# Kernel tuning notes

Measured on AMD Instinct MI355X. Metric: run time of the kernel, lower is better.

The kernel has to match this reference:

```python
import jax, jax.numpy as jnp
import numpy as np

WS = 8            # window size
OWIN = 12         # overlapping window: int(8*0.5)+8
HEADS = 4
DHEAD = 16
INNER = 64        # HEADS*DHEAD
DIM = 48
B, H, W = 4, 192, 192
HN, WN = H // WS, W // WS
NW = HN * WN
NK = NW // 2      # deterministic hard-token keep count (ratio=0.5, E[gumbel rate]=0.5)
SCALE = DHEAD ** -0.5


def conv1x1(x, w, b=None):
    y = jnp.einsum('bchw,oc->bohw', x, w)
    return y if b is None else y + b[:, None, None]


def win_part(x):
    # 'b c (h dh) (w dw) -> b (h w) (dh dw) c'
    b, c, h, w = x.shape
    x = x.reshape(b, c, h // WS, WS, w // WS, WS).transpose(0, 2, 4, 3, 5, 1)
    return x.reshape(b, (h // WS) * (w // WS), WS * WS, c)


def win_unpart(x, h, w):
    b, n, l, c = x.shape
    x = x.reshape(b, h // WS, w // WS, WS, WS, c).transpose(0, 5, 1, 3, 2, 4)
    return x.reshape(b, c, h, w)


def unfold_overlap(x):
    # nn.Unfold(kernel=OWIN, stride=WS, pad=(OWIN-WS)//2) -> (b, NW, OWIN^2, c)
    pad = (OWIN - WS) // 2
    xp = jnp.pad(x, ((0, 0), (0, 0), (pad, pad), (pad, pad)))
    hi = (jnp.arange(HN) * WS)[:, None] + jnp.arange(OWIN)[None]
    wi = (jnp.arange(WN) * WS)[:, None] + jnp.arange(OWIN)[None]
    p = xp[:, :, hi[:, None, :, None], wi[None, :, None, :]]  # (b,c,HN,WN,OWIN,OWIN)
    b, c = x.shape[:2]
    return p.reshape(b, c, NW, OWIN * OWIN).transpose(0, 2, 3, 1)


def rel_to_abs(x):
    b, l, m = x.shape
    r = (m + 1) // 2
    x = jnp.pad(x, ((0, 0), (0, 0), (0, 1)))
    flat = jnp.pad(x.reshape(b, l * (m + 1)), ((0, 0), (0, m - l)))
    return flat.reshape(b, l + 1, m)[:, :l, m - r:]


def relative_logits_1d(q, rel_k):
    b, h, w, d = q.shape
    r = (rel_k.shape[0] + 1) // 2
    logits = jnp.einsum('bxyd,rd->bxyr', q, rel_k)
    logits = rel_to_abs(logits.reshape(b * h, w, -1)).reshape(b, h, w, r)
    return jnp.broadcast_to(logits[:, :, None, :, :], (b, h, r, w, r))


def rel_pos_emb(q, rel_h, rel_w):
    # q: (B_, WS*WS, d) -> (B_, WS*WS, OWIN*OWIN)
    B_, L, d = q.shape
    q4 = q.reshape(B_, WS, WS, d)
    lw = relative_logits_1d(q4, rel_w).transpose(0, 1, 3, 2, 4).reshape(B_, L, -1)
    lh = relative_logits_1d(q4.transpose(0, 2, 1, 3), rel_h).transpose(0, 3, 1, 4, 2).reshape(B_, L, -1)
    return lw + lh


def reference(x, condition_global, wq, bq, wk, bk, wv, bv, w_in, b_in, ln_w, ln_b,
              w_sa, b_sa, w_m1, b_m1, w_m2, b_m2, rel_h, rel_w, w_out, b_out):
    b = x.shape[0]
    qs = conv1x1(x, wq, bq)
    ks = conv1x1(x, wk, bk)
    vs = conv1x1(x, wv, bv)

    # deformable condition: per-window normalized coordinate grid
    lin = jnp.linspace(-1.0, 1.0, WS, dtype=x.dtype)
    gy, gx = jnp.meshgrid(lin, lin, indexing='ij')
    wind = jnp.tile(jnp.stack([gy, gx]), (1, HN, WN))
    cond = jnp.concatenate([vs, condition_global, jnp.broadcast_to(wind, (b, 2, H, W))], axis=1)

    # PredictorLG (inference routing)
    t = conv1x1(cond, w_in, b_in)
    mu = t.mean(1, keepdims=True)
    var = ((t - mu) ** 2).mean(1, keepdims=True)
    t = (t - mu) / jnp.sqrt(var + 1e-6)
    t = t * ln_w[:, None, None] + ln_b[:, None, None]
    t = jax.nn.leaky_relu(t, 0.1)
    sa = jax.nn.sigmoid(jax.lax.conv_general_dilated(
        t, w_sa, (1, 1), ((1, 1), (1, 1)),
        dimension_numbers=('NCHW', 'OIHW', 'NCHW')) + b_sa[:, None, None])
    m = win_part(t.mean(1, keepdims=True)).reshape(b, NW, WS * WS)
    h1 = jax.nn.leaky_relu(m @ w_m1.T + b_m1, 0.1)
    pred = jax.nn.softmax(h1 @ w_m2.T + b_m2, axis=-1)
    score = pred[:, :, 0]
    order = jnp.argsort(-score, axis=1)
    idx1, idx2 = order[:, :NK], order[:, NK:]

    # hard branch: gather -> overlapping window attention with rel-pos bias
    qw = jnp.take_along_axis(win_part(qs), idx1[:, :, None, None], axis=1)       # (b,NK,WS^2,INNER)
    kw = jnp.take_along_axis(unfold_overlap(ks), idx1[:, :, None, None], axis=1)  # (b,NK,OWIN^2,INNER)
    vw = jnp.take_along_axis(unfold_overlap(vs), idx1[:, :, None, None], axis=1)
    qh = qw.reshape(b, NK, WS * WS, HEADS, DHEAD)
    kh = kw.reshape(b, NK, OWIN * OWIN, HEADS, DHEAD)
    vh = vw.reshape(b, NK, OWIN * OWIN, HEADS, DHEAD)
    sim = SCALE * jnp.einsum('bnqhd,bnkhd->bnhqk', qh, kh)
    rp = rel_pos_emb(qh.transpose(0, 1, 3, 2, 4).reshape(b * NK * HEADS, WS * WS, DHEAD), rel_h, rel_w)
    sim = sim + rp.reshape(b, NK, HEADS, WS * WS, OWIN * OWIN)
    attn = jax.nn.softmax(sim, axis=-1)
    hard = jnp.einsum('bnhqk,bnkhd->bnqhd', attn, vh).reshape(b, NK, WS * WS, INNER)

    # easy branch: spatial-attention-gated values
    easy = jnp.take_along_axis(win_part(vs * sa), idx2[:, :, None, None], axis=1)

    # scatter-merge (batch_index_fill)
    bar = jnp.arange(b)[:, None]
    merged = jnp.zeros((b, NW, WS * WS, INNER), x.dtype)
    merged = merged.at[bar, idx1].set(hard).at[bar, idx2].set(easy)
    out = win_unpart(merged, H, W)
    return conv1x1(out, w_out, b_out)


def setup_inputs() -> dict:
    key = jax.random.key(0)
    k = jax.random.split(key, 16)
    rn = lambda kk, s, sc=0.05: jax.random.normal(kk, s, jnp.float32) * sc
    return {
        'x': jax.random.normal(k[0], (B, DIM, H, W), jnp.float32),
        'condition_global': jax.random.normal(k[1], (B, 2, H, W), jnp.float32),
        'wq': rn(k[2], (INNER, DIM)), 'bq': jnp.zeros((INNER,), jnp.float32),
        'wk': rn(k[3], (INNER, DIM)), 'bk': jnp.zeros((INNER,), jnp.float32),
        'wv': rn(k[4], (INNER, DIM)), 'bv': jnp.zeros((INNER,), jnp.float32),
        'w_in': rn(k[5], (17, 68)), 'b_in': jnp.zeros((17,), jnp.float32),
        'ln_w': jnp.ones((17,), jnp.float32), 'ln_b': jnp.zeros((17,), jnp.float32),
        'w_sa': rn(k[6], (1, 17, 3, 3)), 'b_sa': jnp.zeros((1,), jnp.float32),
        'w_m1': rn(k[7], (WS, WS * WS)), 'b_m1': jnp.zeros((WS,), jnp.float32),
        'w_m2': rn(k[8], (2, WS)), 'b_m2': jnp.zeros((2,), jnp.float32),
        'rel_h': rn(k[9], (2 * OWIN - 1, DHEAD), DHEAD ** -0.5),
        'rel_w': rn(k[10], (2 * OWIN - 1, DHEAD), DHEAD ** -0.5),
        'w_out': rn(k[11], (DIM, INNER)), 'b_out': jnp.zeros((DIM,), jnp.float32),
    }
```

## Files before the change

### kernel.cpp

```cpp
#include <hip/hip_runtime.h>
#include <math.h>

#define Hh 192
#define Ww 192
#define HWc 36864
#define Bc 4
#define NWc 576
#define NKc 288
#define WNc 24

typedef _Float16 h2_t __attribute__((ext_vector_type(2)));
typedef _Float16 f16x4 __attribute__((ext_vector_type(4)));
typedef float f32x4 __attribute__((ext_vector_type(4)));
typedef unsigned u32x2 __attribute__((ext_vector_type(2)));
__device__ __forceinline__ h2_t u2h(unsigned u) { return __builtin_bit_cast(h2_t, u); }
__device__ __forceinline__ unsigned h2u(h2_t h) { return __builtin_bit_cast(unsigned, h); }
__device__ __forceinline__ h2_t pkrtz(float a, float b) {
    return __builtin_bit_cast(h2_t, __builtin_amdgcn_cvt_pkrtz(a, b));
}
__device__ __forceinline__ f16x4 pk4(float4 v) {
    u32x2 p = { h2u(pkrtz(v.x, v.y)), h2u(pkrtz(v.z, v.w)) };
    return __builtin_bit_cast(f16x4, p);
}
#define L2E 1.44269504f

__global__ __launch_bounds__(256, 1) void k_qkv(const float* __restrict__ x,
    const float* __restrict__ wq, const float* __restrict__ bq,
    const float* __restrict__ wk, const float* __restrict__ bk,
    const float* __restrict__ wvw, const float* __restrict__ bv,
    _Float16* __restrict__ q, _Float16* __restrict__ k, float* __restrict__ v)
{
    __shared__ float xs[132][52];

    int tid = threadIdx.x;
    int blk = blockIdx.x;
    int b = blk / 288;
    int g0 = (blk % 288) * 128;
    const float* xb = x + (size_t)b * 48 * HWc + g0;

    #pragma unroll
    for (int it = 0; it < 24; ++it) {
        int i = it * 256 + tid;
        int c = i >> 7, px = i & 127;
        xs[px][c] = xb[(size_t)c * HWc + px];
    }

    int ln = tid & 63, wave = tid >> 6;
    int dgrp = ln >> 4;
    __syncthreads();

    size_t pbase = (size_t)b * HWc + g0;

    {
        f16x4 Aq[4][3], Ak[4][3];
        #pragma unroll
        for (int ot = 0; ot < 4; ++ot)
            #pragma unroll
            for (int ks = 0; ks < 3; ++ks) {
                int oc = ot * 16 + (ln & 15);
                Aq[ot][ks] = pk4(*(const float4*)(wq + oc * 48 + ks * 16 + dgrp * 4));
                Ak[ot][ks] = pk4(*(const float4*)(wk + oc * 48 + ks * 16 + dgrp * 4));
            }
        float4 bqf[4], bkf[4];
        #pragma unroll
        for (int ot = 0; ot < 4; ++ot) {
            bqf[ot] = *(const float4*)(bq + ot * 16 + dgrp * 4);
            bkf[ot] = *(const float4*)(bk + ot * 16 + dgrp * 4);
        }

        #pragma unroll
        for (int t2 = 0; t2 < 2; ++t2) {
            int tn = wave * 2 + t2;
            int px = tn * 16 + (ln & 15);
            f16x4 Bf[3];
            #pragma unroll
            for (int ks = 0; ks < 3; ++ks)
                Bf[ks] = pk4(*(const float4*)&xs[px][ks * 16 + dgrp * 4]);

            #pragma unroll
            for (int ot = 0; ot < 4; ++ot) {
                f32x4 Dq = { bqf[ot].x, bqf[ot].y, bqf[ot].z, bqf[ot].w };
                f32x4 Dk = { bkf[ot].x, bkf[ot].y, bkf[ot].z, bkf[ot].w };
                #pragma unroll
                for (int ks = 0; ks < 3; ++ks) {
                    Dq = __builtin_amdgcn_mfma_f32_16x16x16f16(Aq[ot][ks], Bf[ks], Dq, 0, 0, 0);
                    Dk = __builtin_amdgcn_mfma_f32_16x16x16f16(Ak[ot][ks], Bf[ks], Dk, 0, 0, 0);
                }
                u32x2 q2 = { h2u(pkrtz(Dq[0], Dq[1])), h2u(pkrtz(Dq[2], Dq[3])) };
                u32x2 k2 = { h2u(pkrtz(Dk[0], Dk[1])), h2u(pkrtz(Dk[2], Dk[3])) };
                size_t off = (pbase + (size_t)px) * 64 + ot * 16 + dgrp * 4;
                *(u32x2*)(q + off) = q2;
                *(u32x2*)(k + off) = k2;
            }
        }
    }

    {
        float4 Wv[12];
        #pragma unroll
        for (int j = 0; j < 12; ++j) Wv[j] = *(const float4*)(wvw + ln * 48 + j * 4);
        float bvv = bv[ln];

        int p0 = wave * 32;
        #pragma unroll 1
        for (int g4 = 0; g4 < 8; ++g4) {
            int px = p0 + g4 * 4;
            float a0 = bvv, a1 = bvv, a2 = bvv, a3 = bvv;
            #pragma unroll
            for (int j = 0; j < 12; ++j) {
                float4 x0 = *(const float4*)&xs[px + 0][j * 4];
                float4 x1 = *(const float4*)&xs[px + 1][j * 4];
                float4 x2 = *(const float4*)&xs[px + 2][j * 4];
                float4 x3 = *(const float4*)&xs[px + 3][j * 4];
                a0 = fmaf(x0.x, Wv[j].x, a0); a0 = fmaf(x0.y, Wv[j].y, a0);
                a0 = fmaf(x0.z, Wv[j].z, a0); a0 = fmaf(x0.w, Wv[j].w, a0);
                a1 = fmaf(x1.x, Wv[j].x, a1); a1 = fmaf(x1.y, Wv[j].y, a1);
                a1 = fmaf(x1.z, Wv[j].z, a1); a1 = fmaf(x1.w, Wv[j].w, a1);
                a2 = fmaf(x2.x, Wv[j].x, a2); a2 = fmaf(x2.y, Wv[j].y, a2);
                a2 = fmaf(x2.z, Wv[j].z, a2); a2 = fmaf(x2.w, Wv[j].w, a2);
                a3 = fmaf(x3.x, Wv[j].x, a3); a3 = fmaf(x3.y, Wv[j].y, a3);
                a3 = fmaf(x3.z, Wv[j].z, a3); a3 = fmaf(x3.w, Wv[j].w, a3);
            }
            v[(pbase + (size_t)(px + 0)) * 64 + ln] = a0;
            v[(pbase + (size_t)(px + 1)) * 64 + ln] = a1;
            v[(pbase + (size_t)(px + 2)) * 64 + ln] = a2;
            v[(pbase + (size_t)(px + 3)) * 64 + ln] = a3;
        }
    }
}

__global__ __launch_bounds__(256) void k_cond(const float* __restrict__ vs,
    const float* __restrict__ cg,
    const float* __restrict__ w_in, const float* __restrict__ b_in,
    const float* __restrict__ ln_w, const float* __restrict__ ln_b,
    float* __restrict__ t, float* __restrict__ mpix)
{
    int g = blockIdx.x * 256 + threadIdx.x;
    int b = g / HWc, rem = g % HWc;
    int y = rem / Ww, xx = rem % Ww;

    float in[68];
    const float* vp = vs + (size_t)g * 64;
    #pragma unroll
    for (int c = 0; c < 64; c += 4) {
        float4 t4 = *(const float4*)(vp + c);
        in[c] = t4.x; in[c+1] = t4.y; in[c+2] = t4.z; in[c+3] = t4.w;
    }
    in[64] = cg[((size_t)b * 2 + 0) * HWc + rem];
    in[65] = cg[((size_t)b * 2 + 1) * HWc + rem];
    const float step = 2.0f / 7.0f;
    in[66] = -1.0f + step * (float)(y & 7);
    in[67] = -1.0f + step * (float)(xx & 7);

    float tv[17];
    float mu = 0.f;
    #pragma unroll
    for (int o = 0; o < 17; ++o) {
        float a = b_in[o];
        const float* wr = w_in + o * 68;
        #pragma unroll
        for (int c = 0; c < 68; ++c) a = fmaf(in[c], wr[c], a);
        tv[o] = a;
        mu += a;
    }
    mu *= (1.f / 17.f);
    float var = 0.f;
    #pragma unroll
    for (int o = 0; o < 17; ++o) { float d = tv[o] - mu; var = fmaf(d, d, var); }
    var *= (1.f / 17.f);
    float rstd = 1.f / sqrtf(var + 1e-6f);

    float msum = 0.f;
    #pragma unroll
    for (int o = 0; o < 17; ++o) {
        float z = (tv[o] - mu) * rstd * ln_w[o] + ln_b[o];
        z = (z >= 0.f) ? z : 0.1f * z;
        t[((size_t)b * 17 + o) * HWc + rem] = z;
        msum += z;
    }
    mpix[(size_t)b * HWc + rem] = msum * (1.f / 17.f);
}

__global__ __launch_bounds__(256) void k_sa(const float* __restrict__ t,
    const float* __restrict__ w_sa, const float* __restrict__ b_sa,
    float* __restrict__ sa)
{
    int g = blockIdx.x * 256 + threadIdx.x;
    int b = g / HWc, rem = g % HWc;
    int y = rem / Ww, xx = rem % Ww;

    float a = b_sa[0];
    for (int c = 0; c < 17; ++c) {
        const float* tp = t + ((size_t)b * 17 + c) * HWc;
        const float* wr = w_sa + c * 9;
        #pragma unroll
        for (int ki = 0; ki < 3; ++ki) {
            int yy = y + ki - 1;
            if ((unsigned)yy >= 192u) continue;
            #pragma unroll
            for (int kj = 0; kj < 3; ++kj) {
                int xc = xx + kj - 1;
                if ((unsigned)xc >= 192u) continue;
                a = fmaf(tp[yy * Ww + xc], wr[ki * 3 + kj], a);
            }
        }
    }
    sa[g] = 1.f / (1.f + expf(-a));
}

__global__ __launch_bounds__(576) void k_score(const float* __restrict__ mpix,
    const float* __restrict__ w_m1, const float* __restrict__ b_m1,
    const float* __restrict__ w_m2, const float* __restrict__ b_m2,
    int* __restrict__ hardl, int* __restrict__ easyl)
{
    __shared__ float sc[NWc];
    int b = blockIdx.x;
    int w = threadIdx.x;
    {
        int hy = w / WNc, wx = w % WNc;
        const float* mp = mpix + (size_t)b * HWc + (hy * 8) * Ww + wx * 8;
        float m[64];
        #pragma unroll
        for (int l = 0; l < 64; ++l) m[l] = mp[(l >> 3) * Ww + (l & 7)];
        float h1[8];
        #pragma unroll
        for (int j = 0; j < 8; ++j) {
            float a = b_m1[j];
            const float* wr = w_m1 + j * 64;
            #pragma unroll
            for (int l = 0; l < 64; ++l) a = fmaf(m[l], wr[l], a);
            h1[j] = (a >= 0.f) ? a : 0.1f * a;
        }
        float l0 = b_m2[0], l1 = b_m2[1];
        #pragma unroll
        for (int j = 0; j < 8; ++j) {
            l0 = fmaf(h1[j], w_m2[j], l0);
            l1 = fmaf(h1[j], w_m2[8 + j], l1);
        }
        float mx = fmaxf(l0, l1);
        float e0 = expf(l0 - mx), e1 = expf(l1 - mx);
        sc[w] = e0 / (e0 + e1);
    }
    __syncthreads();
    float s = sc[w];
    int cnt = 0;
    for (int w2 = 0; w2 < NWc; ++w2) {
        float s2 = sc[w2];
        cnt += ((s2 > s) || (s2 == s && w2 < w)) ? 1 : 0;
    }
    if (cnt < NKc) hardl[b * NKc + cnt] = w;
    else           easyl[b * NKc + (cnt - NKc)] = w;
}

__global__ __launch_bounds__(256) void k_hard(const _Float16* __restrict__ qs,
    const _Float16* __restrict__ ks, const float* __restrict__ vsb,
    const int* __restrict__ hardl,
    const float* __restrict__ relh, const float* __restrict__ relw,
    const float* __restrict__ w_out, const float* __restrict__ b_out,
    float* __restrict__ out)
{
    __shared__ __align__(16) unsigned char smem[53760];
    unsigned char* Kl  = smem;
    unsigned char* Vt  = smem + 18432;
    unsigned char* Rel = smem + 37376;
    _Float16 (*mldsh)[72] = (_Float16 (*)[72])smem;

    int tid = threadIdx.x;
    int blk = blockIdx.x;
    int b = blk / NKc;
    int n = hardl[blk];
    int hy = n / WNc, wx = n % WNc;
    int y0 = hy * 8, x0 = wx * 8;

    #pragma unroll
    for (int i = 0; i < 9; ++i) {
        int idx = i * 256 + tid;
        int px = idx >> 4, c4 = idx & 15;
        int py = px / 12, pxx = px - py * 12;
        int ky = y0 - 2 + py, kx = x0 - 2 + pxx;
        bool ok = ((unsigned)ky < 192u) && ((unsigned)kx < 192u);
        int kyc = min(max(ky, 0), 191), kxc = min(max(kx, 0), 191);
        size_t poff = ((size_t)(b * HWc) + kyc * Ww + kxc) * 64 + c4 * 4;
        uint2 k2 = *(const uint2*)(ks + poff);
        float4 v4 = *(const float4*)(vsb + poff);
        if (!ok) { k2 = make_uint2(0, 0); v4 = make_float4(0, 0, 0, 0); }
        int hd = c4 >> 2, d0 = (c4 & 3) * 4;
        *(uint2*)(Kl + hd * 4608 + px * 32 + (c4 & 3) * 8) = k2;
        _Float16* vh = (_Float16*)(Vt + hd * 4736);
        vh[(d0 + 0) * 148 + px] = (_Float16)v4.x;
        vh[(d0 + 1) * 148 + px] = (_Float16)v4.y;
        vh[(d0 + 2) * 148 + px] = (_Float16)v4.z;
        vh[(d0 + 3) * 148 + px] = (_Float16)v4.w;
    }

    int h = __builtin_amdgcn_readfirstlane(tid >> 6);
    int l = tid & 63;
    int dgrp = l >> 4;

    {
        int qr = l >> 3, qc = l & 7;
        const _Float16* qp = qs + ((size_t)(b * HWc) + (y0 + qr) * Ww + (x0 + qc)) * 64 + h * 16;
        uint4 q0 = *(const uint4*)qp;
        uint4 q1 = *(const uint4*)(qp + 8);
        h2_t qhp[8] = { u2h(q0.x), u2h(q0.y), u2h(q0.z), u2h(q0.w),
                        u2h(q1.x), u2h(q1.y), u2h(q1.z), u2h(q1.w) };
        float qv[16];
        #pragma unroll
        for (int j = 0; j < 8; ++j) { qv[2*j] = (float)qhp[j].x; qv[2*j+1] = (float)qhp[j].y; }

        float rw[12], rh[12];
        #pragma unroll
        for (int kc = 0; kc < 12; ++kc) {
            const float* rp = relw + (kc - qc + 11) * 16;
            float a = 0.f;
            #pragma unroll
            for (int j = 0; j < 4; ++j) {
                float4 t4 = *(const float4*)(rp + j * 4);
                a = fmaf(qv[j*4+0], t4.x, a); a = fmaf(qv[j*4+1], t4.y, a);
                a = fmaf(qv[j*4+2], t4.z, a); a = fmaf(qv[j*4+3], t4.w, a);
            }
            rw[kc] = a;
        }
        #pragma unroll
        for (int kr = 0; kr < 12; ++kr) {
            const float* rp = relh + (kr - qr + 11) * 16;
            float a = 0.f;
            #pragma unroll
            for (int j = 0; j < 4; ++j) {
                float4 t4 = *(const float4*)(rp + j * 4);
                a = fmaf(qv[j*4+0], t4.x, a); a = fmaf(qv[j*4+1], t4.y, a);
                a = fmaf(qv[j*4+2], t4.z, a); a = fmaf(qv[j*4+3], t4.w, a);
            }
            rh[kr] = a;
        }
        unsigned rr[16];
        #pragma unroll
        for (int j = 0; j < 6; ++j) rr[j]     = h2u(pkrtz(L2E * rw[2*j], L2E * rw[2*j+1]));
        #pragma unroll
        for (int j = 0; j < 6; ++j) rr[6 + j] = h2u(pkrtz(L2E * rh[2*j], L2E * rh[2*j+1]));
        rr[12] = rr[13] = rr[14] = rr[15] = 0u;
        uint4* dst = (uint4*)(Rel + h * 4096 + l * 64);
        dst[0] = make_uint4(rr[0], rr[1], rr[2],  rr[3]);
        dst[1] = make_uint4(rr[4], rr[5], rr[6],  rr[7]);
        dst[2] = make_uint4(rr[8], rr[9], rr[10], rr[11]);
        dst[3] = make_uint4(rr[12], rr[13], rr[14], rr[15]);
    }
    __syncthreads();

    f16x4 qb[4], rb1[4], rb2[4];
    {
        const h2_t qsc = { (_Float16)(0.25f * L2E), (_Float16)(0.25f * L2E) };
        #pragma unroll
        for (int tn = 0; tn < 4; ++tn) {
            int q = tn * 16 + (l & 15);
            int qr = q >> 3, qc = q & 7;
            uint2 raw = *(const uint2*)(qs + ((size_t)(b * HWc) + (y0 + qr) * Ww + (x0 + qc)) * 64 + h * 16 + dgrp * 4);
            h2_t lo = u2h(raw.x) * qsc, hi = u2h(raw.y) * qsc;
            u32x2 packed = { h2u(lo), h2u(hi) };
            qb[tn] = __builtin_bit_cast(f16x4, packed);
            const unsigned char* rbase = Rel + h * 4096 + q * 64 + dgrp * 8;
            rb1[tn] = *(const f16x4*)rbase;
            rb2[tn] = *(const f16x4*)(rbase + 32);
        }
    }

    f32x4 Oacc[4];
    float lsum[4];
    #pragma unroll
    for (int tn = 0; tn < 4; ++tn) { Oacc[tn] = (f32x4){0.f,0.f,0.f,0.f}; lsum[tn] = 0.f; }
    const f32x4 zf = {0.f, 0.f, 0.f, 0.f};
    const float SH = 3.0f * L2E;

    f16x4 kaA = *(const f16x4*)(Kl + h * 4608 + (l & 15) * 32 + dgrp * 8);
    f16x4 vaA = *(const f16x4*)(Vt + h * 4736 + (l & 15) * 296 + (dgrp * 4) * 2);

    #pragma unroll 1
    for (int tm = 0; tm < 9; ++tm) {
        int tmn = (tm + 1 < 9) ? tm + 1 : 0;
        f16x4 kaB = *(const f16x4*)(Kl + h * 4608 + (tmn * 16 + (l & 15)) * 32 + dgrp * 8);
        f16x4 vaB = *(const f16x4*)(Vt + h * 4736 + (l & 15) * 296 + (tmn * 16 + dgrp * 4) * 2);

        int key = tm * 16 + (l & 15);
        int kr = (key * 2731) >> 15;
        int kc = key - kr * 12;
        f16x4 oh1, oh2;
        #pragma unroll
        for (int i = 0; i < 4; ++i) {
            int a1 = 4 * dgrp + i;
            bool v1 = (a1 < 12) ? (kc == a1) : (kr == a1 - 12);
            oh1[i] = v1 ? (_Float16)1.0f : (_Float16)0.0f;
            int a2 = 16 + 4 * dgrp + i;
            bool v2 = (a2 < 24) && (kr == a2 - 12);
            oh2[i] = v2 ? (_Float16)1.0f : (_Float16)0.0f;
        }

        #pragma unroll
        for (int tn = 0; tn < 4; ++tn) {
            f32x4 s = __builtin_amdgcn_mfma_f32_16x16x16f16(kaA, qb[tn],  zf, 0, 0, 0);
            s       = __builtin_amdgcn_mfma_f32_16x16x16f16(oh1, rb1[tn], s,  0, 0, 0);
            s       = __builtin_amdgcn_mfma_f32_16x16x16f16(oh2, rb2[tn], s,  0, 0, 0);
            float e0 = exp2f(s[0] - SH);
            float e1 = exp2f(s[1] - SH);
            float e2 = exp2f(s[2] - SH);
            float e3 = exp2f(s[3] - SH);
            lsum[tn] += (e0 + e1) + (e2 + e3);
            u32x2 pp = { h2u(pkrtz(e0, e1)), h2u(pkrtz(e2, e3)) };
            f16x4 pb = __builtin_bit_cast(f16x4, pp);
            Oacc[tn] = __builtin_amdgcn_mfma_f32_16x16x16f16(vaA, pb, Oacc[tn], 0, 0, 0);
        }
        kaA = kaB; vaA = vaB;
    }

    __syncthreads();
    #pragma unroll
    for (int tn = 0; tn < 4; ++tn) {
        float s = lsum[tn];
        s += __shfl_xor(s, 16);
        s += __shfl_xor(s, 32);
        float inv = 1.f / s;
        int q = tn * 16 + (l & 15);
        u32x2 w2 = { h2u(pkrtz(Oacc[tn][0] * inv, Oacc[tn][1] * inv)),
                     h2u(pkrtz(Oacc[tn][2] * inv, Oacc[tn][3] * inv)) };
        *(u32x2*)&mldsh[q][h * 16 + dgrp * 4] = w2;
    }
    __syncthreads();

    {
        int tn2 = h;
        int pxl = tn2 * 16 + (l & 15);
        f16x4 bf[4];
        #pragma unroll
        for (int ks = 0; ks < 4; ++ks)
            bf[ks] = *(const f16x4*)&mldsh[pxl][ks * 16 + dgrp * 4];

        int gy = y0 + (pxl >> 3), gx = x0 + (pxl & 7);
        #pragma unroll
        for (int ot = 0; ot < 3; ++ot) {
            float4 bi = *(const float4*)(b_out + ot * 16 + dgrp * 4);
            f32x4 Cacc = { bi.x, bi.y, bi.z, bi.w };
            #pragma unroll
            for (int ks = 0; ks < 4; ++ks) {
                float4 wv = *(const float4*)(w_out + (ot * 16 + (l & 15)) * 64 + ks * 16 + dgrp * 4);
                Cacc = __builtin_amdgcn_mfma_f32_16x16x16f16(pk4(wv), bf[ks], Cacc, 0, 0, 0);
            }
            #pragma unroll
            for (int i = 0; i < 4; ++i)
                out[((size_t)(b * 48 + ot * 16 + dgrp * 4 + i)) * HWc + gy * Ww + gx] = Cacc[i];
        }
    }
}

__global__ __launch_bounds__(256) void k_easy(const float* __restrict__ vsb,
    const float* __restrict__ sab, const int* __restrict__ easyl,
    const float* __restrict__ w_out, const float* __restrict__ b_out,
    float* __restrict__ out)
{
    __shared__ __align__(16) _Float16 mldsh[64][72];

    int tid = threadIdx.x;
    int blk = blockIdx.x;
    int b = blk / NKc;
    int n = easyl[blk];
    int hy = n / WNc, wx = n % WNc;
    int y0 = hy * 8, x0 = wx * 8;

    {
        int l = tid >> 2, part = tid & 3;
        int gy = y0 + (l >> 3), gx = x0 + (l & 7);
        const float* vp = vsb + ((size_t)(b * HWc) + gy * Ww + gx) * 64 + part * 16;
        float sv = sab[(size_t)b * HWc + gy * Ww + gx];
        #pragma unroll
        for (int j = 0; j < 4; ++j) {
            float4 v4 = *(const float4*)(vp + j * 4);
            u32x2 w2 = { h2u(pkrtz(v4.x * sv, v4.y * sv)),
                         h2u(pkrtz(v4.z * sv, v4.w * sv)) };
            *(u32x2*)&mldsh[l][part * 16 + j * 4] = w2;
        }
    }
    __syncthreads();

    {
        int l = tid & 63;
        int tn2 = __builtin_amdgcn_readfirstlane(tid >> 6);
        int dgrp = l >> 4;
        int pxl = tn2 * 16 + (l & 15);
        f16x4 bf[4];
        #pragma unroll
        for (int ks = 0; ks < 4; ++ks)
            bf[ks] = *(const f16x4*)&mldsh[pxl][ks * 16 + dgrp * 4];

        int gy = y0 + (pxl >> 3), gx = x0 + (pxl & 7);
        #pragma unroll
        for (int ot = 0; ot < 3; ++ot) {
            float4 bi = *(const float4*)(b_out + ot * 16 + dgrp * 4);
            f32x4 Cacc = { bi.x, bi.y, bi.z, bi.w };
            #pragma unroll
            for (int ks = 0; ks < 4; ++ks) {
                float4 wv = *(const float4*)(w_out + (ot * 16 + (l & 15)) * 64 + ks * 16 + dgrp * 4);
                Cacc = __builtin_amdgcn_mfma_f32_16x16x16f16(pk4(wv), bf[ks], Cacc, 0, 0, 0);
            }
            #pragma unroll
            for (int i = 0; i < 4; ++i)
                out[((size_t)(b * 48 + ot * 16 + dgrp * 4 + i)) * HWc + gy * Ww + gx] = Cacc[i];
        }
    }
}

extern "C" void kernel_launch(void* const* d_in, const int* in_sizes, int n_in,
                              void* d_out, int out_size, void* d_ws, size_t ws_size,
                              hipStream_t stream)
{
    const float* x    = (const float*)d_in[0];
    const float* cg   = (const float*)d_in[1];
    const float* wq   = (const float*)d_in[2];
    const float* bq   = (const float*)d_in[3];
    const float* wk   = (const float*)d_in[4];
    const float* bk   = (const float*)d_in[5];
    const float* wv   = (const float*)d_in[6];
    const float* bv   = (const float*)d_in[7];
    const float* w_in = (const float*)d_in[8];
    const float* b_in = (const float*)d_in[9];
    const float* ln_w = (const float*)d_in[10];
    const float* ln_b = (const float*)d_in[11];
    const float* w_sa = (const float*)d_in[12];
    const float* b_sa = (const float*)d_in[13];
    const float* w_m1 = (const float*)d_in[14];
    const float* b_m1 = (const float*)d_in[15];
    const float* w_m2 = (const float*)d_in[16];
    const float* b_m2 = (const float*)d_in[17];
    const float* rel_h= (const float*)d_in[18];
    const float* rel_w= (const float*)d_in[19];
    const float* w_out= (const float*)d_in[20];
    const float* b_out= (const float*)d_in[21];
    float* out = (float*)d_out;

    _Float16* qsh = (_Float16*)d_ws;
    _Float16* ksh = qsh + (size_t)Bc * 64 * HWc;
    float* vs   = (float*)(ksh + (size_t)Bc * 64 * HWc);
    float* t    = vs + (size_t)Bc * 64 * HWc;
    float* sa   = t  + (size_t)Bc * 17 * HWc;
    float* mpix = sa + (size_t)Bc * HWc;
    int*   hardl= (int*)(mpix + (size_t)Bc * HWc);
    int*   easyl= hardl + Bc * NKc;

    k_qkv  <<<1152, 256, 0, stream>>>(x, wq, bq, wk, bk, wv, bv, qsh, ksh, vs);
    k_cond <<<576, 256, 0, stream>>>(vs, cg, w_in, b_in, ln_w, ln_b, t, mpix);
    k_sa   <<<576, 256, 0, stream>>>(t, w_sa, b_sa, sa);
    k_score<<<4, 576, 0, stream>>>(mpix, w_m1, b_m1, w_m2, b_m2, hardl, easyl);
    k_easy <<<1152, 256, 0, stream>>>(vs, sa, easyl, w_out, b_out, out);
    k_hard <<<1152, 256, 0, stream>>>(qsh, ksh, vs, hardl, rel_h, rel_w, w_out, b_out, out);
}
```

Baseline: 202.2 us.

## Fuse condition projection and 3x3 spatial-attention conv into one row kernel

Merges k_cond and k_sa into a single kernel with one block per image row. Each block recomputes the 17-channel layernormed condition features for rows y-1, y and y+1 into shared memory, then applies the 3x3 conv and sigmoid from LDS. This removes the global write and read of the 17-channel intermediate and one launch. In exchange the 68x17 projection is computed three times per pixel, reading vs three times.

```diff
diff --git a/kernel.cpp b/kernel.cpp
--- a/kernel.cpp
+++ b/kernel.cpp
@@ -129,69 +129,73 @@
     }
 }
 
-__global__ __launch_bounds__(256) void k_cond(const float* __restrict__ vs,
+__global__ __launch_bounds__(192) void k_condsa(const float* __restrict__ vs,
     const float* __restrict__ cg,
     const float* __restrict__ w_in, const float* __restrict__ b_in,
     const float* __restrict__ ln_w, const float* __restrict__ ln_b,
-    float* __restrict__ t, float* __restrict__ mpix)
+    const float* __restrict__ w_sa, const float* __restrict__ b_sa,
+    float* __restrict__ sa, float* __restrict__ mpix)
 {
-    int g = blockIdx.x * 256 + threadIdx.x;
-    int b = g / HWc, rem = g % HWc;
-    int y = rem / Ww, xx = rem % Ww;
-
-    float in[68];
-    const float* vp = vs + (size_t)g * 64;
-    #pragma unroll
-    for (int c = 0; c < 64; c += 4) {
-        float4 t4 = *(const float4*)(vp + c);
-        in[c] = t4.x; in[c+1] = t4.y; in[c+2] = t4.z; in[c+3] = t4.w;
-    }
-    in[64] = cg[((size_t)b * 2 + 0) * HWc + rem];
-    in[65] = cg[((size_t)b * 2 + 1) * HWc + rem];
+    __shared__ float tl[3][17][194];
+
+    int px = threadIdx.x;
+    int blk = blockIdx.x;
+    int b = blk / Hh;
+    int y = blk % Hh;
     const float step = 2.0f / 7.0f;
-    in[66] = -1.0f + step * (float)(y & 7);
-    in[67] = -1.0f + step * (float)(xx & 7);
-
-    float tv[17];
-    float mu = 0.f;
-    #pragma unroll
-    for (int o = 0; o < 17; ++o) {
-        float a = b_in[o];
-        const float* wr = w_in + o * 68;
-        #pragma unroll
-        for (int c = 0; c < 68; ++c) a = fmaf(in[c], wr[c], a);
-        tv[o] = a;
-        mu += a;
-    }
-    mu *= (1.f / 17.f);
-    float var = 0.f;
-    #pragma unroll
-    for (int o = 0; o < 17; ++o) { float d = tv[o] - mu; var = fmaf(d, d, var); }
-    var *= (1.f / 17.f);
-    float rstd = 1.f / sqrtf(var + 1e-6f);
-
-    float msum = 0.f;
-    #pragma unroll
-    for (int o = 0; o < 17; ++o) {
-        float z = (tv[o] - mu) * rstd * ln_w[o] + ln_b[o];
-        z = (z >= 0.f) ? z : 0.1f * z;
-        t[((size_t)b * 17 + o) * HWc + rem] = z;
-        msum += z;
-    }
-    mpix[(size_t)b * HWc + rem] = msum * (1.f / 17.f);
-}
-
-__global__ __launch_bounds__(256) void k_sa(const float* __restrict__ t,
-    const float* __restrict__ w_sa, const float* __restrict__ b_sa,
-    float* __restrict__ sa)
-{
-    int g = blockIdx.x * 256 + threadIdx.x;
-    int b = g / HWc, rem = g % HWc;
-    int y = rem / Ww, xx = rem % Ww;
+    float gx_in = -1.0f + step * (float)(px & 7);
+
+    #pragma unroll 1
+    for (int r = 0; r < 3; ++r) {
+        int yy = y - 1 + r;
+        if ((unsigned)yy >= 192u) continue;
+        size_t prem = (size_t)yy * Ww + px;
+
+        float in[68];
+        const float* vp = vs + ((size_t)b * HWc + prem) * 64;
+        #pragma unroll
+        for (int c = 0; c < 64; c += 4) {
+            float4 t4 = *(const float4*)(vp + c);
+            in[c] = t4.x; in[c+1] = t4.y; in[c+2] = t4.z; in[c+3] = t4.w;
+        }
+        in[64] = cg[((size_t)b * 2 + 0) * HWc + prem];
+        in[65] = cg[((size_t)b * 2 + 1) * HWc + prem];
+        in[66] = -1.0f + step * (float)(yy & 7);
+        in[67] = gx_in;
+
+        float tv[17];
+        float mu = 0.f;
+        #pragma unroll
+        for (int o = 0; o < 17; ++o) {
+            float a = b_in[o];
+            const float* wr = w_in + o * 68;
+            #pragma unroll
+            for (int c = 0; c < 68; ++c) a = fmaf(in[c], wr[c], a);
+            tv[o] = a;
+            mu += a;
+        }
+        mu *= (1.f / 17.f);
+        float var = 0.f;
+        #pragma unroll
+        for (int o = 0; o < 17; ++o) { float d = tv[o] - mu; var = fmaf(d, d, var); }
+        var *= (1.f / 17.f);
+        float rstd = 1.f / sqrtf(var + 1e-6f);
+
+        float msum = 0.f;
+        #pragma unroll
+        for (int o = 0; o < 17; ++o) {
+            float z = (tv[o] - mu) * rstd * ln_w[o] + ln_b[o];
+            z = (z >= 0.f) ? z : 0.1f * z;
+            tl[r][o][px] = z;
+            msum += z;
+        }
+        if (r == 1) mpix[(size_t)b * HWc + prem] = msum * (1.f / 17.f);
+    }
+    __syncthreads();
 
     float a = b_sa[0];
+    #pragma unroll 1
     for (int c = 0; c < 17; ++c) {
-        const float* tp = t + ((size_t)b * 17 + c) * HWc;
         const float* wr = w_sa + c * 9;
         #pragma unroll
         for (int ki = 0; ki < 3; ++ki) {
@@ -199,13 +203,13 @@
             if ((unsigned)yy >= 192u) continue;
             #pragma unroll
             for (int kj = 0; kj < 3; ++kj) {
-                int xc = xx + kj - 1;
+                int xc = px + kj - 1;
                 if ((unsigned)xc >= 192u) continue;
-                a = fmaf(tp[yy * Ww + xc], wr[ki * 3 + kj], a);
-            }
-        }
-    }
-    sa[g] = 1.f / (1.f + expf(-a));
+                a = fmaf(tl[ki][c][xc], wr[ki * 3 + kj], a);
+            }
+        }
+    }
+    sa[(size_t)b * HWc + (size_t)y * Ww + px] = 1.f / (1.f + expf(-a));
 }
 
 __global__ __launch_bounds__(576) void k_score(const float* __restrict__ mpix,
@@ -537,16 +541,14 @@
     _Float16* qsh = (_Float16*)d_ws;
     _Float16* ksh = qsh + (size_t)Bc * 64 * HWc;
     float* vs   = (float*)(ksh + (size_t)Bc * 64 * HWc);
-    float* t    = vs + (size_t)Bc * 64 * HWc;
-    float* sa   = t  + (size_t)Bc * 17 * HWc;
+    float* sa   = vs + (size_t)Bc * 64 * HWc;
     float* mpix = sa + (size_t)Bc * HWc;
     int*   hardl= (int*)(mpix + (size_t)Bc * HWc);
     int*   easyl= hardl + Bc * NKc;
 
-    k_qkv  <<<1152, 256, 0, stream>>>(x, wq, bq, wk, bk, wv, bv, qsh, ksh, vs);
-    k_cond <<<576, 256, 0, stream>>>(vs, cg, w_in, b_in, ln_w, ln_b, t, mpix);
-    k_sa   <<<576, 256, 0, stream>>>(t, w_sa, b_sa, sa);
-    k_score<<<4, 576, 0, stream>>>(mpix, w_m1, b_m1, w_m2, b_m2, hardl, easyl);
-    k_easy <<<1152, 256, 0, stream>>>(vs, sa, easyl, w_out, b_out, out);
-    k_hard <<<1152, 256, 0, stream>>>(qsh, ksh, vs, hardl, rel_h, rel_w, w_out, b_out, out);
-}
+    k_qkv   <<<1152, 256, 0, stream>>>(x, wq, bq, wk, bk, wv, bv, qsh, ksh, vs);
+    k_condsa<<<Bc * Hh, 192, 0, stream>>>(vs, cg, w_in, b_in, ln_w, ln_b, w_sa, b_sa, sa, mpix);
+    k_score <<<4, 576, 0, stream>>>(mpix, w_m1, b_m1, w_m2, b_m2, hardl, easyl);
+    k_easy  <<<1152, 256, 0, stream>>>(vs, sa, easyl, w_out, b_out, out);
+    k_hard  <<<1152, 256, 0, stream>>>(qsh, ksh, vs, hardl, rel_h, rel_w, w_out, b_out, out);
+}
```

Result: faster. 193.5 us (-4.3%).
